# Performance work log

Hardware: AMD Instinct MI355X
Metric: run time of the kernel (lower is better)

The kernel has to match this reference:

```python
import jax, jax.numpy as jnp
import numpy as np

H = 128

def _rnn_layer(inp, W_ih, W_hh, b_ih, b_hh):
    # inp: [B, T, D]; precompute the input projection for all timesteps at once
    pre = jnp.einsum('btd,hd->bth', inp, W_ih) + b_ih + b_hh  # [B, T, H]
    B = inp.shape[0]
    h0 = jnp.zeros((B, H), dtype=inp.dtype)

    def step(h, p_t):  # p_t: [B, H]
        h_new = jnp.tanh(p_t + h @ W_hh.T)
        return h_new, h_new

    _, hs = jax.lax.scan(step, h0, jnp.swapaxes(pre, 0, 1))  # [T, B, H]
    return jnp.swapaxes(hs, 0, 1)  # [B, T, H]


def setup_inputs() -> dict:
    key = jax.random.key(0)
    ks = jax.random.split(key, 12)
    B, T, D = 64, 512, 2048
    s_in = 1.0 / np.sqrt(H)  # PyTorch RNN init scale ~ U(-1/sqrt(H), 1/sqrt(H))
    u = lambda k, shape: jax.random.uniform(k, shape, jnp.float32, -s_in, s_in)
    return {
        'x': jax.random.normal(ks[0], (B, T, D), jnp.float32),
        'W_ih1': u(ks[1], (H, D)),
        'W_hh1': u(ks[2], (H, H)),
        'b_ih1': u(ks[3], (H,)),
        'b_hh1': u(ks[4], (H,)),
        'W_ih2': u(ks[5], (H, H)),
        'W_hh2': u(ks[6], (H, H)),
        'b_ih2': u(ks[7], (H,)),
        'b_hh2': u(ks[8], (H,)),
        'W_fc': u(ks[9], (1, H)),
        'b_fc': u(ks[10], (1,)),
    }


def reference(x, W_ih1, W_hh1, b_ih1, b_hh1, W_ih2, W_hh2, b_ih2, b_hh2, W_fc, b_fc):
    h1 = _rnn_layer(x, W_ih1, W_hh1, b_ih1, b_hh1)   # [B, T, H]
    h2 = _rnn_layer(h1, W_ih2, W_hh2, b_ih2, b_hh2)  # [B, T, H]
    last = h2[:, -1, :]                               # [B, H]
    return last @ W_fc.T + b_fc                       # [B, 1]
```

## Files before the change

kernel.cpp:

```cpp
#include <hip/hip_runtime.h>
#include <cstddef>
#include <cstdint>

#define BB 64
#define TT 512
#define DD 2048
#define HH 128
#define M1 (BB*TT)

typedef __attribute__((ext_vector_type(8))) short bf16x8;
typedef __attribute__((ext_vector_type(4))) float f32x4;
typedef __attribute__((ext_vector_type(2))) _Float16 h2f;

__device__ __forceinline__ unsigned short f2bf(float f) {
    unsigned u = __builtin_bit_cast(unsigned, f);
    u += 0x7fffu + ((u >> 16) & 1u);
    return (unsigned short)(u >> 16);
}
__device__ __forceinline__ float bf2f(unsigned short s) {
    return __builtin_bit_cast(float, ((unsigned)s) << 16);
}
__device__ __forceinline__ float tanh_fast(float x) {
    float e2x = __builtin_amdgcn_exp2f(x * 2.885390081777927f);
    return 1.0f - 2.0f * __builtin_amdgcn_rcpf(e2x + 1.0f);
}

__global__ __launch_bounds__(256) void prep_w_kernel(
    const float* __restrict__ W,
    unsigned short* __restrict__ Whi, unsigned short* __restrict__ Wlo)
{
    const int i = (blockIdx.x * 256 + threadIdx.x) * 4;
    float4 w = *(const float4*)(W + i);
    unsigned short h0 = f2bf(w.x), h1 = f2bf(w.y), h2 = f2bf(w.z), h3 = f2bf(w.w);
    unsigned short l0 = f2bf(w.x - bf2f(h0)), l1 = f2bf(w.y - bf2f(h1));
    unsigned short l2 = f2bf(w.z - bf2f(h2)), l3 = f2bf(w.w - bf2f(h3));
    ushort4 hv; hv.x = h0; hv.y = h1; hv.z = h2; hv.w = h3;
    ushort4 lv; lv.x = l0; lv.y = l1; lv.z = l2; lv.w = l3;
    *(ushort4*)(Whi + i) = hv;
    *(ushort4*)(Wlo + i) = lv;
}

__global__ __launch_bounds__(256) void gemm1_mfma_kernel(
    const float* __restrict__ A, const unsigned short* __restrict__ Whi,
    const unsigned short* __restrict__ Wlo,
    const float* __restrict__ bia, const float* __restrict__ bib,
    float* __restrict__ out)
{
    constexpr int K = DD, BK = 32, NK = K / BK;
    __shared__ __align__(16) short Ah[64 * 40];
    __shared__ __align__(16) short Al[64 * 40];
    __shared__ __align__(16) short Wh[128 * 40];
    __shared__ __align__(16) short Wl[128 * 40];

    const int tid = threadIdx.x, wave = tid >> 6, lane = tid & 63;
    const size_t m0 = (size_t)blockIdx.x * 64;
    const int ar = tid >> 2, ak = (tid & 3) * 8;
    const int wr = tid >> 1, wk = (tid & 1) * 16;
    const float* Ap = A + (m0 + ar) * (size_t)K + ak;
    const unsigned short* Whp = Whi + (size_t)wr * K + wk;
    const unsigned short* Wlp = Wlo + (size_t)wr * K + wk;
    const int frow = lane & 15, fko = (lane >> 4) * 8;

    f32x4 acc[8];
#pragma unroll
    for (int i = 0; i < 8; i++) acc[i] = (f32x4){0.f, 0.f, 0.f, 0.f};

    for (int kt = 0; kt < NK; ++kt) {
        float4 a0 = *(const float4*)(Ap + kt * BK);
        float4 a1 = *(const float4*)(Ap + kt * BK + 4);
        bf16x8 wh0 = *(const bf16x8*)(Whp + kt * BK);
        bf16x8 wh1 = *(const bf16x8*)(Whp + kt * BK + 8);
        bf16x8 wl0 = *(const bf16x8*)(Wlp + kt * BK);
        bf16x8 wl1 = *(const bf16x8*)(Wlp + kt * BK + 8);
        __syncthreads();
        float fv[8] = {a0.x, a0.y, a0.z, a0.w, a1.x, a1.y, a1.z, a1.w};
        unsigned short h[8], l[8];
#pragma unroll
        for (int i = 0; i < 8; i++) {
            h[i] = f2bf(fv[i]);
            l[i] = f2bf(fv[i] - bf2f(h[i]));
        }
        uint2 p0, p1, q0, q1;
        p0.x = (unsigned)h[0] | ((unsigned)h[1] << 16); p0.y = (unsigned)h[2] | ((unsigned)h[3] << 16);
        p1.x = (unsigned)h[4] | ((unsigned)h[5] << 16); p1.y = (unsigned)h[6] | ((unsigned)h[7] << 16);
        q0.x = (unsigned)l[0] | ((unsigned)l[1] << 16); q0.y = (unsigned)l[2] | ((unsigned)l[3] << 16);
        q1.x = (unsigned)l[4] | ((unsigned)l[5] << 16); q1.y = (unsigned)l[6] | ((unsigned)l[7] << 16);
        *(uint2*)&Ah[ar * 40 + ak]     = p0;
        *(uint2*)&Ah[ar * 40 + ak + 4] = p1;
        *(uint2*)&Al[ar * 40 + ak]     = q0;
        *(uint2*)&Al[ar * 40 + ak + 4] = q1;
        *(bf16x8*)&Wh[wr * 40 + wk]     = wh0;
        *(bf16x8*)&Wh[wr * 40 + wk + 8] = wh1;
        *(bf16x8*)&Wl[wr * 40 + wk]     = wl0;
        *(bf16x8*)&Wl[wr * 40 + wk + 8] = wl1;
        __syncthreads();
        bf16x8 fAh = *(const bf16x8*)&Ah[(wave * 16 + frow) * 40 + fko];
        bf16x8 fAl = *(const bf16x8*)&Al[(wave * 16 + frow) * 40 + fko];
#pragma unroll
        for (int nt = 0; nt < 8; ++nt) {
            bf16x8 fWh = *(const bf16x8*)&Wh[(nt * 16 + frow) * 40 + fko];
            bf16x8 fWl = *(const bf16x8*)&Wl[(nt * 16 + frow) * 40 + fko];
            acc[nt] = __builtin_amdgcn_mfma_f32_16x16x32_bf16(fAh, fWh, acc[nt], 0, 0, 0);
            acc[nt] = __builtin_amdgcn_mfma_f32_16x16x32_bf16(fAh, fWl, acc[nt], 0, 0, 0);
            acc[nt] = __builtin_amdgcn_mfma_f32_16x16x32_bf16(fAl, fWh, acc[nt], 0, 0, 0);
        }
    }
    const int rbase = (lane >> 4) * 4;
#pragma unroll
    for (int nt = 0; nt < 8; ++nt) {
        const int col = nt * 16 + frow;
        const float bv = bia[col] + bib[col];
#pragma unroll
        for (int r = 0; r < 4; r++)
            out[(m0 + wave * 16 + rbase + r) * HH + col] = acc[nt][r] + bv;
    }
}

template<int K>
__global__ __launch_bounds__(256) void gemm_bias_kernel(
    const float* __restrict__ A, const float* __restrict__ W,
    const float* __restrict__ bia, const float* __restrict__ bib,
    float* __restrict__ out)
{
    constexpr int BM = 64, BK = 16;
    constexpr int NK = K / BK;
    __shared__ float As[BK][68];
    __shared__ float Bs[BK][132];
    const int tid = threadIdx.x;
    const int tc = tid & 15, tr = tid >> 4;
    const size_t m0 = (size_t)blockIdx.x * BM;
    const int arow = tid >> 2, ak4 = (tid & 3) * 4;
    const int bn0 = tid >> 1, bk = (tid & 1) * 8;
    const float* Aptr = A + (m0 + arow) * (size_t)K + ak4;
    const float* Wptr = W + (size_t)bn0 * K + bk;
    float4 ra = *(const float4*)Aptr;
    float4 rb0 = *(const float4*)(Wptr);
    float4 rb1 = *(const float4*)(Wptr + 4);
    float acc[4][8];
#pragma unroll
    for (int i = 0; i < 4; i++)
#pragma unroll
        for (int j = 0; j < 8; j++) acc[i][j] = 0.0f;
    for (int kt = 0; kt < NK; ++kt) {
        __syncthreads();
        As[ak4 + 0][arow] = ra.x; As[ak4 + 1][arow] = ra.y;
        As[ak4 + 2][arow] = ra.z; As[ak4 + 3][arow] = ra.w;
        Bs[bk + 0][bn0] = rb0.x; Bs[bk + 1][bn0] = rb0.y;
        Bs[bk + 2][bn0] = rb0.z; Bs[bk + 3][bn0] = rb0.w;
        Bs[bk + 4][bn0] = rb1.x; Bs[bk + 5][bn0] = rb1.y;
        Bs[bk + 6][bn0] = rb1.z; Bs[bk + 7][bn0] = rb1.w;
        __syncthreads();
        if (kt + 1 < NK) {
            ra = *(const float4*)(Aptr + (size_t)(kt + 1) * BK);
            rb0 = *(const float4*)(Wptr + (size_t)(kt + 1) * BK);
            rb1 = *(const float4*)(Wptr + (size_t)(kt + 1) * BK + 4);
        }
#pragma unroll
        for (int kk = 0; kk < BK; ++kk) {
            const float4 av = *(const float4*)&As[kk][tr * 4];
            const float4 b0 = *(const float4*)&Bs[kk][tc * 4];
            const float4 b1 = *(const float4*)&Bs[kk][64 + tc * 4];
            const float aa[4] = {av.x, av.y, av.z, av.w};
            const float bb[8] = {b0.x, b0.y, b0.z, b0.w, b1.x, b1.y, b1.z, b1.w};
#pragma unroll
            for (int i = 0; i < 4; i++)
#pragma unroll
                for (int j = 0; j < 8; j++)
                    acc[i][j] = __builtin_fmaf(aa[i], bb[j], acc[i][j]);
        }
    }
    float bs[8];
#pragma unroll
    for (int j = 0; j < 4; j++) {
        bs[j] = bia[tc * 4 + j] + bib[tc * 4 + j];
        bs[j + 4] = bia[64 + tc * 4 + j] + bib[64 + tc * 4 + j];
    }
#pragma unroll
    for (int i = 0; i < 4; i++) {
        const size_t r = m0 + tr * 4 + i;
        float4 o0 = {acc[i][0] + bs[0], acc[i][1] + bs[1], acc[i][2] + bs[2], acc[i][3] + bs[3]};
        float4 o1 = {acc[i][4] + bs[4], acc[i][5] + bs[5], acc[i][6] + bs[6], acc[i][7] + bs[7]};
        *(float4*)&out[r * HH + tc * 4] = o0;
        *(float4*)&out[r * HH + 64 + tc * 4] = o1;
    }
}

__global__ __launch_bounds__(64) void rnn_scan_f16(
    const float* __restrict__ pre,
    const float* __restrict__ Whh,
    float* __restrict__ hout,
    const float* __restrict__ Wfc, const float* __restrict__ bfc,
    float* __restrict__ outv,
    const int store_h)
{
    __shared__ __align__(16) _Float16 hsf[HH];
    const int l = threadIdx.x;
    const int b = blockIdx.x;

    h2f W0[64], W1[64];
    {
        const float* r0 = Whh + l * HH;
        const float* r1 = Whh + (l + 64) * HH;
#pragma unroll
        for (int q = 0; q < 32; q++) {
            float4 w = *(const float4*)(r0 + q * 4);
            W0[2 * q]     = h2f{(_Float16)w.x, (_Float16)w.y};
            W0[2 * q + 1] = h2f{(_Float16)w.z, (_Float16)w.w};
            float4 v = *(const float4*)(r1 + q * 4);
            W1[2 * q]     = h2f{(_Float16)v.x, (_Float16)v.y};
            W1[2 * q + 1] = h2f{(_Float16)v.z, (_Float16)v.w};
        }
    }
    hsf[l] = (_Float16)0.f;
    hsf[l + 64] = (_Float16)0.f;

    const float* pb = pre + (size_t)b * TT * HH;
    float* hob = hout + (size_t)b * TT * HH;
    float pn0 = pb[l], pn1 = pb[l + 64];
    float fc0 = 0.f;

    for (int t = 0; t < TT; ++t) {
        const float p0 = pn0, p1 = pn1;
        if (t + 1 < TT) {
            pn0 = pb[(size_t)(t + 1) * HH + l];
            pn1 = pb[(size_t)(t + 1) * HH + l + 64];
        }
        float a0 = 0.f, a0b = 0.f, a1 = 0.f, a1b = 0.f;
#pragma unroll
        for (int q = 0; q < 16; q++) {
            uint4 hv = *(const uint4*)&hsf[q * 8];
            h2f x0 = __builtin_bit_cast(h2f, hv.x);
            h2f x1 = __builtin_bit_cast(h2f, hv.y);
            h2f x2 = __builtin_bit_cast(h2f, hv.z);
            h2f x3 = __builtin_bit_cast(h2f, hv.w);
            a0  = __builtin_amdgcn_fdot2(W0[4 * q],     x0, a0,  false);
            a0b = __builtin_amdgcn_fdot2(W0[4 * q + 1], x1, a0b, false);
            a0  = __builtin_amdgcn_fdot2(W0[4 * q + 2], x2, a0,  false);
            a0b = __builtin_amdgcn_fdot2(W0[4 * q + 3], x3, a0b, false);
            a1  = __builtin_amdgcn_fdot2(W1[4 * q],     x0, a1,  false);
            a1b = __builtin_amdgcn_fdot2(W1[4 * q + 1], x1, a1b, false);
            a1  = __builtin_amdgcn_fdot2(W1[4 * q + 2], x2, a1,  false);
            a1b = __builtin_amdgcn_fdot2(W1[4 * q + 3], x3, a1b, false);
        }
        const float h0 = tanh_fast(p0 + a0 + a0b);
        const float h1 = tanh_fast(p1 + a1 + a1b);
        hsf[l] = (_Float16)h0;
        hsf[l + 64] = (_Float16)h1;
        if (store_h) {
            hob[(size_t)t * HH + l] = h0;
            hob[(size_t)t * HH + l + 64] = h1;
        }
        if (t == TT - 1) fc0 = h0 * Wfc[l] + h1 * Wfc[l + 64];
    }

    if (!store_h) {
#pragma unroll
        for (int off = 1; off < 64; off <<= 1) fc0 += __shfl_xor(fc0, off);
        if (l == 0) outv[b] = fc0 + bfc[0];
    }
}

extern "C" void kernel_launch(void* const* d_in, const int* in_sizes, int n_in,
                              void* d_out, int out_size, void* d_ws, size_t ws_size,
                              hipStream_t stream) {
    const float* x    = (const float*)d_in[0];
    const float* Wih1 = (const float*)d_in[1];
    const float* Whh1 = (const float*)d_in[2];
    const float* bih1 = (const float*)d_in[3];
    const float* bhh1 = (const float*)d_in[4];
    const float* Wih2 = (const float*)d_in[5];
    const float* Whh2 = (const float*)d_in[6];
    const float* bih2 = (const float*)d_in[7];
    const float* bhh2 = (const float*)d_in[8];
    const float* Wfc  = (const float*)d_in[9];
    const float* bfc  = (const float*)d_in[10];
    float* out = (float*)d_out;

    float* preA = (float*)d_ws;
    float* h1b  = preA + (size_t)M1 * HH;
    unsigned short* Whi = (unsigned short*)h1b;
    unsigned short* Wlo = Whi + (size_t)HH * DD;

    prep_w_kernel<<<dim3(HH * DD / 1024), dim3(256), 0, stream>>>(Wih1, Whi, Wlo);
    gemm1_mfma_kernel<<<dim3(M1 / 64), dim3(256), 0, stream>>>(x, Whi, Wlo, bih1, bhh1, preA);
    rnn_scan_f16<<<dim3(BB), dim3(64), 0, stream>>>(preA, Whh1, h1b, Wfc, bfc, out, 1);
    gemm_bias_kernel<HH><<<dim3(M1 / 64), dim3(256), 0, stream>>>(h1b, Wih2, bih2, bhh2, preA);
    rnn_scan_f16<<<dim3(BB), dim3(64), 0, stream>>>(preA, Whh2, h1b, Wfc, bfc, out, 0);
}
```

Measured before the change: 936.5 us.

## Fuse layer-2 input projection into layer-1 scan and split recurrence across 4 waves

The recurrent scan now runs with 256 threads per batch row. Each output unit is handled by a lane pair that splits K in half and combines the halves with a cross-lane shuffle, using a double-buffered LDS hidden state and one block barrier per step. The layer-1 scan also computes the layer-2 input projection (Wih2·h + biases) in f16 dot products and writes it straight out. This removes the separate fp32 GEMM launch and the h1 store/reload round trip. The cost is a __syncthreads every timestep and fp16 precision for the second projection.

```diff
diff --git a/kernel.cpp b/kernel.cpp
--- a/kernel.cpp
+++ b/kernel.cpp
@@ -116,147 +116,109 @@
     }
 }
 
-template<int K>
-__global__ __launch_bounds__(256) void gemm_bias_kernel(
-    const float* __restrict__ A, const float* __restrict__ W,
-    const float* __restrict__ bia, const float* __restrict__ bib,
-    float* __restrict__ out)
-{
-    constexpr int BM = 64, BK = 16;
-    constexpr int NK = K / BK;
-    __shared__ float As[BK][68];
-    __shared__ float Bs[BK][132];
-    const int tid = threadIdx.x;
-    const int tc = tid & 15, tr = tid >> 4;
-    const size_t m0 = (size_t)blockIdx.x * BM;
-    const int arow = tid >> 2, ak4 = (tid & 3) * 4;
-    const int bn0 = tid >> 1, bk = (tid & 1) * 8;
-    const float* Aptr = A + (m0 + arow) * (size_t)K + ak4;
-    const float* Wptr = W + (size_t)bn0 * K + bk;
-    float4 ra = *(const float4*)Aptr;
-    float4 rb0 = *(const float4*)(Wptr);
-    float4 rb1 = *(const float4*)(Wptr + 4);
-    float acc[4][8];
-#pragma unroll
-    for (int i = 0; i < 4; i++)
-#pragma unroll
-        for (int j = 0; j < 8; j++) acc[i][j] = 0.0f;
-    for (int kt = 0; kt < NK; ++kt) {
-        __syncthreads();
-        As[ak4 + 0][arow] = ra.x; As[ak4 + 1][arow] = ra.y;
-        As[ak4 + 2][arow] = ra.z; As[ak4 + 3][arow] = ra.w;
-        Bs[bk + 0][bn0] = rb0.x; Bs[bk + 1][bn0] = rb0.y;
-        Bs[bk + 2][bn0] = rb0.z; Bs[bk + 3][bn0] = rb0.w;
-        Bs[bk + 4][bn0] = rb1.x; Bs[bk + 5][bn0] = rb1.y;
-        Bs[bk + 6][bn0] = rb1.z; Bs[bk + 7][bn0] = rb1.w;
-        __syncthreads();
-        if (kt + 1 < NK) {
-            ra = *(const float4*)(Aptr + (size_t)(kt + 1) * BK);
-            rb0 = *(const float4*)(Wptr + (size_t)(kt + 1) * BK);
-            rb1 = *(const float4*)(Wptr + (size_t)(kt + 1) * BK + 4);
-        }
-#pragma unroll
-        for (int kk = 0; kk < BK; ++kk) {
-            const float4 av = *(const float4*)&As[kk][tr * 4];
-            const float4 b0 = *(const float4*)&Bs[kk][tc * 4];
-            const float4 b1 = *(const float4*)&Bs[kk][64 + tc * 4];
-            const float aa[4] = {av.x, av.y, av.z, av.w};
-            const float bb[8] = {b0.x, b0.y, b0.z, b0.w, b1.x, b1.y, b1.z, b1.w};
-#pragma unroll
-            for (int i = 0; i < 4; i++)
-#pragma unroll
-                for (int j = 0; j < 8; j++)
-                    acc[i][j] = __builtin_fmaf(aa[i], bb[j], acc[i][j]);
-        }
-    }
-    float bs[8];
-#pragma unroll
-    for (int j = 0; j < 4; j++) {
-        bs[j] = bia[tc * 4 + j] + bib[tc * 4 + j];
-        bs[j + 4] = bia[64 + tc * 4 + j] + bib[64 + tc * 4 + j];
-    }
-#pragma unroll
-    for (int i = 0; i < 4; i++) {
-        const size_t r = m0 + tr * 4 + i;
-        float4 o0 = {acc[i][0] + bs[0], acc[i][1] + bs[1], acc[i][2] + bs[2], acc[i][3] + bs[3]};
-        float4 o1 = {acc[i][4] + bs[4], acc[i][5] + bs[5], acc[i][6] + bs[6], acc[i][7] + bs[7]};
-        *(float4*)&out[r * HH + tc * 4] = o0;
-        *(float4*)&out[r * HH + 64 + tc * 4] = o1;
-    }
-}
-
-__global__ __launch_bounds__(64) void rnn_scan_f16(
+template<int FUSE_NEXT>
+__global__ __launch_bounds__(256) void rnn_scan4_fused(
     const float* __restrict__ pre,
     const float* __restrict__ Whh,
-    float* __restrict__ hout,
+    const float* __restrict__ Wih2,
+    const float* __restrict__ bi2, const float* __restrict__ bh2,
+    float* __restrict__ pre2,
     const float* __restrict__ Wfc, const float* __restrict__ bfc,
-    float* __restrict__ outv,
-    const int store_h)
+    float* __restrict__ outv)
 {
-    __shared__ __align__(16) _Float16 hsf[HH];
-    const int l = threadIdx.x;
-    const int b = blockIdx.x;
-
-    h2f W0[64], W1[64];
+    __shared__ __align__(16) _Float16 hs[2][HH];
+    __shared__ float red[4];
+    const int tid  = threadIdx.x;
+    const int wave = tid >> 6, lane = tid & 63;
+    const int j  = wave * 32 + (lane & 31);
+    const int kh = lane >> 5;
+    const int b  = blockIdx.x;
+
+    h2f Wr[32];
     {
-        const float* r0 = Whh + l * HH;
-        const float* r1 = Whh + (l + 64) * HH;
-#pragma unroll
-        for (int q = 0; q < 32; q++) {
-            float4 w = *(const float4*)(r0 + q * 4);
-            W0[2 * q]     = h2f{(_Float16)w.x, (_Float16)w.y};
-            W0[2 * q + 1] = h2f{(_Float16)w.z, (_Float16)w.w};
-            float4 v = *(const float4*)(r1 + q * 4);
-            W1[2 * q]     = h2f{(_Float16)v.x, (_Float16)v.y};
-            W1[2 * q + 1] = h2f{(_Float16)v.z, (_Float16)v.w};
-        }
-    }
-    hsf[l] = (_Float16)0.f;
-    hsf[l + 64] = (_Float16)0.f;
+        const float* r = Whh + (size_t)j * HH + kh * 64;
+#pragma unroll
+        for (int q = 0; q < 16; q++) {
+            float4 w = *(const float4*)(r + q * 4);
+            Wr[2 * q]     = h2f{(_Float16)w.x, (_Float16)w.y};
+            Wr[2 * q + 1] = h2f{(_Float16)w.z, (_Float16)w.w};
+        }
+    }
+    h2f W2r[32];
+    float bias2 = 0.f;
+    if (FUSE_NEXT) {
+        const float* r = Wih2 + (size_t)j * HH + kh * 64;
+#pragma unroll
+        for (int q = 0; q < 16; q++) {
+            float4 w = *(const float4*)(r + q * 4);
+            W2r[2 * q]     = h2f{(_Float16)w.x, (_Float16)w.y};
+            W2r[2 * q + 1] = h2f{(_Float16)w.z, (_Float16)w.w};
+        }
+        bias2 = bi2[j] + bh2[j];
+    }
+    if (tid < HH) hs[0][tid] = (_Float16)0.f;
 
     const float* pb = pre + (size_t)b * TT * HH;
-    float* hob = hout + (size_t)b * TT * HH;
-    float pn0 = pb[l], pn1 = pb[l + 64];
-    float fc0 = 0.f;
+    float* p2b = FUSE_NEXT ? (pre2 + (size_t)b * TT * HH) : nullptr;
+    float pn0 = pb[j];
+    float pn1 = pb[(size_t)HH + j];
+    float fcv = 0.f;
+    __syncthreads();
 
     for (int t = 0; t < TT; ++t) {
-        const float p0 = pn0, p1 = pn1;
-        if (t + 1 < TT) {
-            pn0 = pb[(size_t)(t + 1) * HH + l];
-            pn1 = pb[(size_t)(t + 1) * HH + l + 64];
-        }
-        float a0 = 0.f, a0b = 0.f, a1 = 0.f, a1b = 0.f;
-#pragma unroll
-        for (int q = 0; q < 16; q++) {
-            uint4 hv = *(const uint4*)&hsf[q * 8];
+        const float p = pn0;
+        pn0 = pn1;
+        if (t + 2 < TT) pn1 = pb[(size_t)(t + 2) * HH + j];
+        const int rb = t & 1;
+        const int wb = rb ^ 1;
+        const _Float16* hp = &hs[rb][kh * 64];
+        float a0 = 0.f, a1 = 0.f, a2 = 0.f, a3 = 0.f;
+#pragma unroll
+        for (int q = 0; q < 8; q++) {
+            uint4 hv = *(const uint4*)(hp + q * 8);
             h2f x0 = __builtin_bit_cast(h2f, hv.x);
             h2f x1 = __builtin_bit_cast(h2f, hv.y);
             h2f x2 = __builtin_bit_cast(h2f, hv.z);
             h2f x3 = __builtin_bit_cast(h2f, hv.w);
-            a0  = __builtin_amdgcn_fdot2(W0[4 * q],     x0, a0,  false);
-            a0b = __builtin_amdgcn_fdot2(W0[4 * q + 1], x1, a0b, false);
-            a0  = __builtin_amdgcn_fdot2(W0[4 * q + 2], x2, a0,  false);
-            a0b = __builtin_amdgcn_fdot2(W0[4 * q + 3], x3, a0b, false);
-            a1  = __builtin_amdgcn_fdot2(W1[4 * q],     x0, a1,  false);
-            a1b = __builtin_amdgcn_fdot2(W1[4 * q + 1], x1, a1b, false);
-            a1  = __builtin_amdgcn_fdot2(W1[4 * q + 2], x2, a1,  false);
-            a1b = __builtin_amdgcn_fdot2(W1[4 * q + 3], x3, a1b, false);
-        }
-        const float h0 = tanh_fast(p0 + a0 + a0b);
-        const float h1 = tanh_fast(p1 + a1 + a1b);
-        hsf[l] = (_Float16)h0;
-        hsf[l + 64] = (_Float16)h1;
-        if (store_h) {
-            hob[(size_t)t * HH + l] = h0;
-            hob[(size_t)t * HH + l + 64] = h1;
-        }
-        if (t == TT - 1) fc0 = h0 * Wfc[l] + h1 * Wfc[l + 64];
-    }
-
-    if (!store_h) {
-#pragma unroll
-        for (int off = 1; off < 64; off <<= 1) fc0 += __shfl_xor(fc0, off);
-        if (l == 0) outv[b] = fc0 + bfc[0];
+            a0 = __builtin_amdgcn_fdot2(Wr[4 * q],     x0, a0, false);
+            a1 = __builtin_amdgcn_fdot2(Wr[4 * q + 1], x1, a1, false);
+            a2 = __builtin_amdgcn_fdot2(Wr[4 * q + 2], x2, a2, false);
+            a3 = __builtin_amdgcn_fdot2(Wr[4 * q + 3], x3, a3, false);
+        }
+        float s = (a0 + a1) + (a2 + a3);
+        s += __shfl_xor(s, 32);
+        const float h = tanh_fast(p + s);
+        if (lane < 32) hs[wb][j] = (_Float16)h;
+        if (!FUSE_NEXT && t == TT - 1 && lane < 32) fcv = h * Wfc[j];
+        __syncthreads();
+
+        if (FUSE_NEXT) {
+            const _Float16* h2p = &hs[wb][kh * 64];
+            float c0 = 0.f, c1 = 0.f, c2 = 0.f, c3 = 0.f;
+#pragma unroll
+            for (int q = 0; q < 8; q++) {
+                uint4 hv = *(const uint4*)(h2p + q * 8);
+                h2f x0 = __builtin_bit_cast(h2f, hv.x);
+                h2f x1 = __builtin_bit_cast(h2f, hv.y);
+                h2f x2 = __builtin_bit_cast(h2f, hv.z);
+                h2f x3 = __builtin_bit_cast(h2f, hv.w);
+                c0 = __builtin_amdgcn_fdot2(W2r[4 * q],     x0, c0, false);
+                c1 = __builtin_amdgcn_fdot2(W2r[4 * q + 1], x1, c1, false);
+                c2 = __builtin_amdgcn_fdot2(W2r[4 * q + 2], x2, c2, false);
+                c3 = __builtin_amdgcn_fdot2(W2r[4 * q + 3], x3, c3, false);
+            }
+            float s2 = (c0 + c1) + (c2 + c3);
+            s2 += __shfl_xor(s2, 32);
+            if (lane < 32) p2b[(size_t)t * HH + j] = s2 + bias2;
+        }
+    }
+
+    if (!FUSE_NEXT) {
+#pragma unroll
+        for (int off = 1; off < 64; off <<= 1) fcv += __shfl_xor(fcv, off);
+        if (lane == 0) red[wave] = fcv;
+        __syncthreads();
+        if (tid == 0) outv[b] = red[0] + red[1] + red[2] + red[3] + bfc[0];
     }
 }
 
@@ -277,13 +239,14 @@
     float* out = (float*)d_out;
 
     float* preA = (float*)d_ws;
-    float* h1b  = preA + (size_t)M1 * HH;
-    unsigned short* Whi = (unsigned short*)h1b;
+    float* preB = preA + (size_t)M1 * HH;
+    unsigned short* Whi = (unsigned short*)preB;
     unsigned short* Wlo = Whi + (size_t)HH * DD;
 
     prep_w_kernel<<<dim3(HH * DD / 1024), dim3(256), 0, stream>>>(Wih1, Whi, Wlo);
     gemm1_mfma_kernel<<<dim3(M1 / 64), dim3(256), 0, stream>>>(x, Whi, Wlo, bih1, bhh1, preA);
-    rnn_scan_f16<<<dim3(BB), dim3(64), 0, stream>>>(preA, Whh1, h1b, Wfc, bfc, out, 1);
-    gemm_bias_kernel<HH><<<dim3(M1 / 64), dim3(256), 0, stream>>>(h1b, Wih2, bih2, bhh2, preA);
-    rnn_scan_f16<<<dim3(BB), dim3(64), 0, stream>>>(preA, Whh2, h1b, Wfc, bfc, out, 0);
-}
+    rnn_scan4_fused<1><<<dim3(BB), dim3(256), 0, stream>>>(
+        preA, Whh1, Wih2, bih2, bhh2, preB, Wfc, bfc, out);
+    rnn_scan4_fused<0><<<dim3(BB), dim3(256), 0, stream>>>(
+        preB, Whh2, nullptr, nullptr, nullptr, nullptr, Wfc, bfc, out);
+}
```

After: 883.2 us. 5.7% less time.
